# Optimization experiments

Hardware: AMD Instinct MI355X
Metric: run time of the kernel (lower is better)

## Reference

```python
import jax, jax.numpy as jnp
import numpy as np

DIM = 1024

def setup_inputs() -> dict:
    key = jax.random.key(0)
    k1, k2, k3, k4, k5 = jax.random.split(key, 5)
    B, S, D = 32, 2048, DIM
    hidden_state = jax.random.normal(k1, (B, D), dtype=jnp.float32)
    encoder_outputs = jax.random.normal(k2, (B, S, D), dtype=jnp.float32)
    # linear1: (2D -> D) with bias; linear2: (D -> 1) no bias
    W1 = jax.random.normal(k3, (2 * D, D), dtype=jnp.float32) / np.sqrt(2 * D)
    b1 = jnp.zeros((D,), dtype=jnp.float32)
    w2 = jax.random.normal(k4, (D,), dtype=jnp.float32) / np.sqrt(D)
    return {"hidden_state": hidden_state, "encoder_outputs": encoder_outputs,
            "W1": W1, "b1": b1, "w2": w2}

def reference(hidden_state, encoder_outputs, W1, b1, w2):
    B, S, D = encoder_outputs.shape
    # concat(encoder_outputs, broadcast hidden) @ W1 == enc @ W1_enc + hid @ W1_hid
    W1_enc, W1_hid = W1[:D], W1[D:]                      # each [D, D]
    enc_proj = jnp.einsum('bsd,de->bse', encoder_outputs, W1_enc)
    hid_proj = jnp.einsum('bd,de->be', hidden_state, W1_hid)
    h = jnp.tanh(enc_proj + hid_proj[:, None, :] + b1)    # [B, S, D]
    e = jnp.einsum('bsd,d->bs', h, w2)                    # [B, S]
    alpha = jax.nn.softmax(e, axis=1)                     # [B, S]
    context = jnp.einsum('bs,bsd->bd', alpha, encoder_outputs)  # [B, D]
    return context
```

## Files before the change

### kernel.cpp

```cpp
#include <hip/hip_runtime.h>
#include <hip/hip_bf16.h>
#include <cstdint>

typedef __bf16 bf16;
typedef __bf16 bf16x8 __attribute__((ext_vector_type(8)));
typedef float  f32x4  __attribute__((ext_vector_type(4)));

#define N_ENCB   0u
#define N_W1BT   134217728u
#define N_C      136314880u
#define N_E      136445952u
#define N_ALPHA  136707072u
#define N_HIDP   136968192u
#define N_CTXP   138016768u
#define N_TOTAL  140113920ull

#define O_W1BT   0u
#define O_C      2097152u
#define O_E      2228224u
#define O_ALPHA  2490368u
#define O_HIDP   2752512u
#define O_CTXP   3801088u

__global__ void k_convert(const float* __restrict__ in, bf16* __restrict__ out) {
    size_t i = ((size_t)blockIdx.x * 256 + threadIdx.x) * 8;
    const size_t stride = (size_t)2048 * 256 * 8;
    for (; i < 67108864ull; i += stride) {
        f32x4 a = *(const f32x4*)(in + i);
        f32x4 b = *(const f32x4*)(in + i + 4);
        bf16x8 o;
        o[0]=(bf16)a[0]; o[1]=(bf16)a[1]; o[2]=(bf16)a[2]; o[3]=(bf16)a[3];
        o[4]=(bf16)b[0]; o[5]=(bf16)b[1]; o[6]=(bf16)b[2]; o[7]=(bf16)b[3];
        *(bf16x8*)(out + i) = o;
    }
}

__global__ void k_cvec_init(const float* __restrict__ b1, float* __restrict__ cvec) {
    int i = blockIdx.x * 256 + threadIdx.x;
    cvec[i] = b1[i & 1023];
}

__global__ void k_hid_atomic(const float* __restrict__ hid, const float* __restrict__ W1,
                             float* __restrict__ cvec) {
    int e = blockIdx.x * 256 + threadIdx.x;
    int dch = blockIdx.y;
    float acc[32];
#pragma unroll
    for (int b = 0; b < 32; ++b) acc[b] = 0.f;
    int d0 = dch * 32;
#pragma unroll 4
    for (int dd = 0; dd < 32; ++dd) {
        int d = d0 + dd;
        float w = W1[(size_t)(1024 + d) * 1024 + e];
#pragma unroll
        for (int b = 0; b < 32; ++b) acc[b] += hid[b * 1024 + d] * w;
    }
#pragma unroll
    for (int b = 0; b < 32; ++b) atomicAdd(&cvec[b * 1024 + e], acc[b]);
}

__global__ void k_hid_partial(const float* __restrict__ hid, const float* __restrict__ W1,
                              float* __restrict__ hidp) {
    int e = blockIdx.x * 256 + threadIdx.x;
    int dch = blockIdx.y;
    float acc[32];
#pragma unroll
    for (int b = 0; b < 32; ++b) acc[b] = 0.f;
    int d0 = dch * 128;
    for (int dd = 0; dd < 128; ++dd) {
        int d = d0 + dd;
        float w = W1[(size_t)(1024 + d) * 1024 + e];
#pragma unroll
        for (int b = 0; b < 32; ++b) acc[b] += hid[b * 1024 + d] * w;
    }
#pragma unroll
    for (int b = 0; b < 32; ++b) hidp[((size_t)dch * 32 + b) * 1024 + e] = acc[b];
}

__global__ void k_hid_reduce(const float* __restrict__ hidp, const float* __restrict__ b1,
                             float* __restrict__ cvec) {
    int i = blockIdx.x * 256 + threadIdx.x;
    int e = i & 1023;
    float s = b1[e];
#pragma unroll
    for (int dch = 0; dch < 8; ++dch) s += hidp[(size_t)dch * 32768 + i];
    cvec[i] = s;
}

__global__ void k_w1t(const float* __restrict__ W1, bf16* __restrict__ w1bt) {
    __shared__ float tile[32][33];
    int tx = threadIdx.x, ty = threadIdx.y;
    int bx = blockIdx.x, by = blockIdx.y;
#pragma unroll
    for (int i = 0; i < 4; ++i)
        tile[ty + i * 8][tx] = W1[(size_t)(by * 32 + ty + i * 8) * 1024 + bx * 32 + tx];
    __syncthreads();
#pragma unroll
    for (int i = 0; i < 4; ++i)
        w1bt[(size_t)(bx * 32 + ty + i * 8) * 1024 + by * 32 + tx] = (bf16)tile[tx][ty + i * 8];
}

__device__ inline float fast_tanh(float x) {
    float e2 = __expf(2.f * x);
    return 1.f - 2.f / (e2 + 1.f);
}

#define SBAR  __builtin_amdgcn_s_barrier()
#define LGKM0 asm volatile("s_waitcnt lgkmcnt(0)" ::: "memory")
#define VMC2  asm volatile("s_waitcnt vmcnt(2)" ::: "memory")
#define VMC4  asm volatile("s_waitcnt vmcnt(4)" ::: "memory")
#define PRIO1 __builtin_amdgcn_s_setprio(1)
#define PRIO0 __builtin_amdgcn_s_setprio(0)

template<int D, int MH>
__device__ __forceinline__ void rdA4(const char* p, bf16x8 (&bA)[4]) {
#pragma unroll
    for (int m = 0; m < 4; ++m)
        bA[m] = *(const bf16x8*)(p + D * 32768 + MH * 8192 + m * 2048);
}
template<int D>
__device__ __forceinline__ void rdB4(const char* p, bf16x8 (&bB)[4]) {
#pragma unroll
    for (int n = 0; n < 4; ++n)
        bB[n] = *(const bf16x8*)(p + D * 32768 + n * 2048);
}
template<int MH>
__device__ __forceinline__ void mfma16(bf16x8 (&bA)[4], bf16x8 (&bB)[4], f32x4 (&acc)[8][4]) {
#pragma unroll
    for (int m = 0; m < 4; ++m)
#pragma unroll
        for (int n = 0; n < 4; ++n)
            acc[MH * 4 + m][n] = __builtin_amdgcn_mfma_f32_16x16x32_bf16(
                bA[m], bB[n], acc[MH * 4 + m][n], 0, 0, 0);
}

__global__ __launch_bounds__(512, 1) void k_gemm8(
    const bf16* __restrict__ encb, const bf16* __restrict__ w1bt,
    const float* __restrict__ cvec, const float* __restrict__ w2,
    float* __restrict__ ebuf)
{
    __shared__ __align__(16) char smem[131072];
    const int t = threadIdx.x;
    const int lane = t & 63;
    const int w  = t >> 6;
    const int wr = w >> 2;
    const int wc = w & 3;
    const int l15 = lane & 15, g = (lane >> 4) & 3;

    unsigned bidx = blockIdx.x;
    unsigned swz0 = (bidx & 7u) * 128u + (bidx >> 3);
    const int nt  = swz0 & 3;
    const int mt0 = swz0 >> 2;
    const int n0  = nt * 256;

    const int r6  = t >> 3;
    const int gsl = (t & 7) ^ (r6 & 7);
    const char* srcA    = (const char*)encb + (size_t)(mt0 * 256 + r6) * 2048 + gsl * 16;
    const char* srcA_nx = srcA + (size_t)2048 * 2048;
    const char* srcB    = (const char*)w1bt + (size_t)(n0 + r6) * 2048 + gsl * 16;

#define STAGE_A(SRC, D, H, KT) do { \
    const char* _s = (SRC) + (size_t)(H) * 262144 + (size_t)(KT) * 128; \
    __builtin_amdgcn_global_load_lds((const __attribute__((address_space(1))) unsigned int*)_s, \
        (__attribute__((address_space(3))) unsigned int*)(smem + (D) * 32768 + (H) * 16384 + w * 1024), 16, 0, 0); \
    __builtin_amdgcn_global_load_lds((const __attribute__((address_space(1))) unsigned int*)(_s + 131072), \
        (__attribute__((address_space(3))) unsigned int*)(smem + (D) * 32768 + (H) * 16384 + 8192 + w * 1024), 16, 0, 0); \
} while (0)
#define STAGE_B(D, H, KT) do { \
    const char* _s = srcB + (size_t)(H) * 262144 + (size_t)(KT) * 128; \
    __builtin_amdgcn_global_load_lds((const __attribute__((address_space(1))) unsigned int*)_s, \
        (__attribute__((address_space(3))) unsigned int*)(smem + 65536 + (D) * 32768 + (H) * 16384 + w * 1024), 16, 0, 0); \
    __builtin_amdgcn_global_load_lds((const __attribute__((address_space(1))) unsigned int*)(_s + 131072), \
        (__attribute__((address_space(3))) unsigned int*)(smem + 65536 + (D) * 32768 + (H) * 16384 + 8192 + w * 1024), 16, 0, 0); \
} while (0)

    const int rbA = wr * 128 + l15;
    const int rbB = wc * 64 + l15;
    const int sK0 = (g ^ (l15 & 7)) << 4;
    const int sK1 = sK0 ^ 64;
    const char* pA0 = smem + rbA * 128 + sK0;
    const char* pA1 = smem + rbA * 128 + sK1;
    const char* pB0 = smem + 65536 + rbB * 128 + sK0;
    const char* pB1 = smem + 65536 + rbB * 128 + sK1;

    f32x4 acc[8][4] = {};
    bf16x8 bA[4], bB[4];

    float wv[4];
    int gcol[4];
#pragma unroll
    for (int n = 0; n < 4; ++n) {
        gcol[n] = n0 + wc * 64 + n * 16 + l15;
        wv[n] = w2[gcol[n]];
    }

    STAGE_A(srcA, 0, 0, 0); STAGE_A(srcA, 0, 1, 0);
    STAGE_B(0, 0, 0); STAGE_B(0, 1, 0);
    STAGE_B(1, 0, 1); STAGE_B(1, 1, 1);
    VMC4; SBAR;

#pragma unroll 1
    for (int j = 0; j < 4; ++j) {
#pragma unroll 1
        for (int i = 0; i < 8; ++i) {
            const int st1 = 2 * i + 1;
            const int st2 = (2 * i + 2) & 15;
            const int st3 = (2 * i + 3) & 15;
            const char* sA2 = (i == 7) ? ((j < 3) ? srcA_nx : srcA) : srcA;

            rdA4<0, 0>(pA0, bA); rdB4<0>(pB0, bB);
            STAGE_A(srcA, 1, 0, st1);
            SBAR; LGKM0; PRIO1; mfma16<0>(bA, bB, acc); PRIO0; SBAR;
            rdA4<0, 1>(pA0, bA);
            STAGE_A(srcA, 1, 1, st1);
            SBAR; LGKM0; PRIO1; mfma16<1>(bA, bB, acc); PRIO0; SBAR;
            rdA4<0, 0>(pA1, bA); rdB4<0>(pB1, bB);
            SBAR; LGKM0; PRIO1; mfma16<0>(bA, bB, acc); PRIO0; SBAR;
            rdA4<0, 1>(pA1, bA);
            STAGE_B(0, 0, st2);
            SBAR; LGKM0; PRIO1; mfma16<1>(bA, bB, acc); PRIO0; VMC2; SBAR;
            rdA4<1, 0>(pA0, bA); rdB4<1>(pB0, bB);
            STAGE_B(0, 1, st2);
            SBAR; LGKM0; PRIO1; mfma16<0>(bA, bB, acc); PRIO0; SBAR;
            rdA4<1, 1>(pA0, bA);
            STAGE_A(sA2, 0, 0, st2);
            SBAR; LGKM0; PRIO1; mfma16<1>(bA, bB, acc); PRIO0; SBAR;
            rdA4<1, 0>(pA1, bA); rdB4<1>(pB1, bB);
            STAGE_A(sA2, 0, 1, st2);
            SBAR; LGKM0; PRIO1; mfma16<0>(bA, bB, acc); PRIO0; SBAR;
            rdA4<1, 1>(pA1, bA);
            STAGE_B(1, 0, st3); STAGE_B(1, 1, st3);
            SBAR; LGKM0; PRIO1; mfma16<1>(bA, bB, acc); PRIO0; VMC4; SBAR;
        }

        const int m0j = (mt0 + 8 * j) * 256;
        const int bj  = m0j >> 11;
        float cv[4];
#pragma unroll
        for (int n = 0; n < 4; ++n) cv[n] = cvec[bj * 1024 + gcol[n]];
#pragma unroll
        for (int m = 0; m < 8; ++m) {
#pragma unroll
            for (int r = 0; r < 4; ++r) {
                float s = 0.f;
#pragma unroll
                for (int n = 0; n < 4; ++n)
                    s += fast_tanh(acc[m][n][r] + cv[n]) * wv[n];
                s += __shfl_xor(s, 1); s += __shfl_xor(s, 2);
                s += __shfl_xor(s, 4); s += __shfl_xor(s, 8);
                if (l15 == 0)
                    atomicAdd(&ebuf[m0j + wr * 128 + m * 16 + g * 4 + r], s);
            }
        }
#pragma unroll
        for (int m = 0; m < 8; ++m)
#pragma unroll
            for (int n = 0; n < 4; ++n)
                acc[m][n] = f32x4{0.f, 0.f, 0.f, 0.f};

        srcA = srcA_nx;
        srcA_nx += (size_t)2048 * 2048;
    }
#undef STAGE_A
#undef STAGE_B
}

__global__ __launch_bounds__(256, 3) void k_gemm_e(
    const float* __restrict__ enc, const bf16* __restrict__ w1bt,
    const float* __restrict__ cvec, const float* __restrict__ w2,
    float* __restrict__ ebuf)
{
    __shared__ __align__(16) unsigned char smem[24 * 1024];
    const int t = threadIdx.x;
    const int lane = t & 63;
    const int w = t >> 6;
    const int wr = w >> 1, wc = w & 1;
    const int l15 = lane & 15, g = lane >> 4;

    unsigned raw = blockIdx.x;
    unsigned swz = (raw & 7u) * 512u + (raw >> 3);
    const int nt = swz & 7, mt = swz >> 3;
    const int m0 = mt * 128, n0 = nt * 128;
    const int b = m0 >> 11;

    int rowA = (t >> 3);
    int slotA = (t & 7) ^ (rowA & 7);
    const char* gA0 = (const char*)enc + (size_t)(m0 + rowA) * 4096 + slotA * 16;
    int rowB = (t >> 2);
    int slotB = (t & 3) ^ ((t >> 3) & 3);
    const char* gB0 = (const char*)w1bt + (size_t)(n0 + rowB) * 2048 + slotB * 16;

    int rowA0 = wr * 64 + l15;
    unsigned offA0 = (unsigned)rowA0 * 128 + ((((2 * g)) ^ (l15 & 7)) << 4);
    int rowB0 = wc * 64 + l15;
    unsigned offB0 = 16384u + (unsigned)rowB0 * 64 + (((g ^ ((l15 >> 1) & 3))) << 4);

    f32x4 acc[4][4] = {};

    for (int kt = 0; kt < 32; ++kt) {
        const char* pa = gA0 + kt * 128;
        const char* pb = gB0 + kt * 64;
#pragma unroll
        for (int c = 0; c < 4; ++c)
            __builtin_amdgcn_global_load_lds(
                (const __attribute__((address_space(1))) unsigned int*)(pa + (size_t)c * 131072),
                (__attribute__((address_space(3))) unsigned int*)(smem + c * 4096 + w * 1024), 16, 0, 0);
#pragma unroll
        for (int c = 0; c < 2; ++c)
            __builtin_amdgcn_global_load_lds(
                (const __attribute__((address_space(1))) unsigned int*)(pb + (size_t)c * 131072),
                (__attribute__((address_space(3))) unsigned int*)(smem + 16384 + c * 4096 + w * 1024), 16, 0, 0);
        __syncthreads();

        bf16x8 af[4], bfr[4];
#pragma unroll
        for (int m = 0; m < 4; ++m) {
            unsigned o0 = offA0 + m * 2048;
            f32x4 lo = *(const f32x4*)(smem + o0);
            f32x4 hi = *(const f32x4*)(smem + (o0 ^ 16u));
            bf16x8 a;
            a[0] = (bf16)lo[0]; a[1] = (bf16)lo[1]; a[2] = (bf16)lo[2]; a[3] = (bf16)lo[3];
            a[4] = (bf16)hi[0]; a[5] = (bf16)hi[1]; a[6] = (bf16)hi[2]; a[7] = (bf16)hi[3];
            af[m] = a;
        }
#pragma unroll
        for (int n = 0; n < 4; ++n)
            bfr[n] = *(const bf16x8*)(smem + (offB0 + n * 1024));
#pragma unroll
        for (int m = 0; m < 4; ++m)
#pragma unroll
            for (int n = 0; n < 4; ++n)
                acc[m][n] = __builtin_amdgcn_mfma_f32_16x16x32_bf16(af[m], bfr[n], acc[m][n], 0, 0, 0);
        __syncthreads();
    }

    float cv[4], wv[4];
#pragma unroll
    for (int n = 0; n < 4; ++n) {
        int gcol = n0 + wc * 64 + n * 16 + l15;
        cv[n] = cvec[b * 1024 + gcol];
        wv[n] = w2[gcol];
    }
#pragma unroll
    for (int m = 0; m < 4; ++m) {
#pragma unroll
        for (int r = 0; r < 4; ++r) {
            float s = 0.f;
#pragma unroll
            for (int n = 0; n < 4; ++n)
                s += fast_tanh(acc[m][n][r] + cv[n]) * wv[n];
            s += __shfl_xor(s, 1); s += __shfl_xor(s, 2);
            s += __shfl_xor(s, 4); s += __shfl_xor(s, 8);
            if (l15 == 0)
                atomicAdd(&ebuf[m0 + wr * 64 + m * 16 + g * 4 + r], s);
        }
    }
}

__global__ void k_softmax(const float* __restrict__ ebuf, float* __restrict__ alpha) {
    int bb = blockIdx.x, t = threadIdx.x;
    __shared__ float red[4], red2[4];
    float v[8];
    float mx = -1e30f;
#pragma unroll
    for (int i = 0; i < 8; ++i) { v[i] = ebuf[bb * 2048 + i * 256 + t]; mx = fmaxf(mx, v[i]); }
    for (int o = 32; o > 0; o >>= 1) mx = fmaxf(mx, __shfl_xor(mx, o));
    if ((t & 63) == 0) red[t >> 6] = mx;
    __syncthreads();
    mx = fmaxf(fmaxf(red[0], red[1]), fmaxf(red[2], red[3]));
    float sum = 0.f;
#pragma unroll
    for (int i = 0; i < 8; ++i) { v[i] = __expf(v[i] - mx); sum += v[i]; }
    for (int o = 32; o > 0; o >>= 1) sum += __shfl_xor(sum, o);
    if ((t & 63) == 0) red2[t >> 6] = sum;
    __syncthreads();
    sum = red2[0] + red2[1] + red2[2] + red2[3];
    float inv = 1.f / sum;
#pragma unroll
    for (int i = 0; i < 8; ++i) alpha[bb * 2048 + i * 256 + t] = v[i] * inv;
}

__global__ void k_ctx_partial_b(const bf16* __restrict__ encb, const float* __restrict__ alpha,
                                float* __restrict__ ctxp) {
    int bid = blockIdx.x;
    int bb = bid >> 4, sc = bid & 15;
    int t = threadIdx.x;
    __shared__ float al[128];
    __shared__ float red[128 * 8];
    if (t < 128) al[t] = alpha[bb * 2048 + sc * 128 + t];
    __syncthreads();
    int d0 = (t & 127) * 8;
    int sp = t >> 7;
    float acc[8] = {};
    const bf16* base = encb + ((size_t)bb * 2048 + sc * 128 + sp) * 1024 + d0;
    for (int s = 0; s < 128; s += 2) {
        bf16x8 v = *(const bf16x8*)(base + (size_t)s * 1024);
        float a = al[s + sp];
#pragma unroll
        for (int k = 0; k < 8; ++k) acc[k] += a * (float)v[k];
    }
    if (sp == 1) {
#pragma unroll
        for (int k = 0; k < 8; ++k) red[(t & 127) * 8 + k] = acc[k];
    }
    __syncthreads();
    if (sp == 0) {
        float* o = ctxp + (size_t)bid * 1024 + d0;
#pragma unroll
        for (int k = 0; k < 8; ++k) o[k] = acc[k] + red[t * 8 + k];
    }
}

__global__ void k_ctx_partial(const float* __restrict__ enc, const float* __restrict__ alpha,
                              float* __restrict__ ctxp) {
    int bid = blockIdx.x;
    int bb = bid >> 4, sc = bid & 15;
    int t = threadIdx.x;
    __shared__ float al[128];
    if (t < 128) al[t] = alpha[bb * 2048 + sc * 128 + t];
    __syncthreads();
    f32x4 acc = {0.f, 0.f, 0.f, 0.f};
    const f32x4* base = (const f32x4*)(enc + ((size_t)bb * 2048 + sc * 128) * 1024) + t;
    for (int s = 0; s < 128; ++s) {
        f32x4 vv = base[(size_t)s * 256];
        acc += vv * al[s];
    }
    *((f32x4*)(ctxp + (size_t)bid * 1024) + t) = acc;
}

__global__ void k_ctx_reduce(const float* __restrict__ ctxp, float* __restrict__ out) {
    int i = blockIdx.x * 256 + threadIdx.x;
    int bb = i >> 10, d = i & 1023;
    float s = 0.f;
#pragma unroll
    for (int sc = 0; sc < 16; ++sc) s += ctxp[((size_t)(bb * 16 + sc)) * 1024 + d];
    out[i] = s;
}

extern "C" void kernel_launch(void* const* d_in, const int* in_sizes, int n_in,
                              void* d_out, int out_size, void* d_ws, size_t ws_size,
                              hipStream_t stream) {
    const float* hid = (const float*)d_in[0];
    const float* enc = (const float*)d_in[1];
    const float* W1  = (const float*)d_in[2];
    const float* b1  = (const float*)d_in[3];
    const float* w2  = (const float*)d_in[4];
    float* out = (float*)d_out;
    char* ws = (char*)d_ws;

    if (ws_size >= N_TOTAL) {
        bf16*  encb  = (bf16*)(ws + N_ENCB);
        bf16*  w1bt  = (bf16*)(ws + N_W1BT);
        float* cvec  = (float*)(ws + N_C);
        float* ebuf  = (float*)(ws + N_E);
        float* alpha = (float*)(ws + N_ALPHA);
        float* ctxp  = (float*)(ws + N_CTXP);

        hipMemsetAsync(ebuf, 0, 65536 * sizeof(float), stream);
        k_convert<<<2048, 256, 0, stream>>>(enc, encb);
        k_w1t<<<dim3(32, 32), dim3(32, 8), 0, stream>>>(W1, w1bt);
        k_cvec_init<<<128, 256, 0, stream>>>(b1, cvec);
        k_hid_atomic<<<dim3(4, 32), 256, 0, stream>>>(hid, W1, cvec);
        k_gemm8<<<256, 512, 0, stream>>>(encb, w1bt, cvec, w2, ebuf);
        k_softmax<<<32, 256, 0, stream>>>(ebuf, alpha);
        k_ctx_partial_b<<<512, 256, 0, stream>>>(encb, alpha, ctxp);
        k_ctx_reduce<<<128, 256, 0, stream>>>(ctxp, out);
    } else {
        bf16*  w1bt  = (bf16*)(ws + O_W1BT);
        float* cvec  = (float*)(ws + O_C);
        float* ebuf  = (float*)(ws + O_E);
        float* alpha = (float*)(ws + O_ALPHA);
        float* hidp  = (float*)(ws + O_HIDP);
        float* ctxp  = (float*)(ws + O_CTXP);

        hipMemsetAsync(ebuf, 0, 65536 * sizeof(float), stream);
        k_hid_partial<<<dim3(4, 8), 256, 0, stream>>>(hid, W1, hidp);
        k_w1t<<<dim3(32, 32), dim3(32, 8), 0, stream>>>(W1, w1bt);
        k_hid_reduce<<<128, 256, 0, stream>>>(hidp, b1, cvec);
        k_gemm_e<<<4096, 256, 0, stream>>>(enc, w1bt, cvec, w2, ebuf);
        k_softmax<<<32, 256, 0, stream>>>(ebuf, alpha);
        k_ctx_partial<<<512, 256, 0, stream>>>(enc, alpha, ctxp);
        k_ctx_reduce<<<128, 256, 0, stream>>>(ctxp, out);
    }
}
```

Measured before the change: 267.0 us.

## Convert encoder outputs into pre-tiled swizzled bf16 layout for contiguous GEMM staging

Replaces the flat fp32-to-bf16 conversion with a kernel that transposes encoder outputs through LDS into a tile-major, XOR-swizzled layout. Each 256-row by 128-byte K-slice is then contiguous, so the GEMM's global-to-LDS A loads read contiguous 16-byte chunks per thread instead of strided rows. The context kernel is rewritten to read the new layout. The aim is better DRAM and cache locality for the A-operand loads, at the cost of a more complex conversion kernel that uses 128KB of LDS per block and so runs at low occupancy.

```diff
diff --git a/kernel.cpp b/kernel.cpp
--- a/kernel.cpp
+++ b/kernel.cpp
@@ -3,10 +3,11 @@
 #include <cstdint>
 
 typedef __bf16 bf16;
+typedef __bf16 bf16x4 __attribute__((ext_vector_type(4)));
 typedef __bf16 bf16x8 __attribute__((ext_vector_type(8)));
 typedef float  f32x4  __attribute__((ext_vector_type(4)));
 
-#define N_ENCB   0u
+#define N_ENCT   0u
 #define N_W1BT   134217728u
 #define N_C      136314880u
 #define N_E      136445952u
@@ -22,16 +23,29 @@
 #define O_HIDP   2752512u
 #define O_CTXP   3801088u
 
-__global__ void k_convert(const float* __restrict__ in, bf16* __restrict__ out) {
-    size_t i = ((size_t)blockIdx.x * 256 + threadIdx.x) * 8;
-    const size_t stride = (size_t)2048 * 256 * 8;
-    for (; i < 67108864ull; i += stride) {
-        f32x4 a = *(const f32x4*)(in + i);
-        f32x4 b = *(const f32x4*)(in + i + 4);
-        bf16x8 o;
-        o[0]=(bf16)a[0]; o[1]=(bf16)a[1]; o[2]=(bf16)a[2]; o[3]=(bf16)a[3];
-        o[4]=(bf16)b[0]; o[5]=(bf16)b[1]; o[6]=(bf16)b[2]; o[7]=(bf16)b[3];
-        *(bf16x8*)(out + i) = o;
+__global__ __launch_bounds__(256) void k_convT(const float* __restrict__ in,
+                                               bf16* __restrict__ encT) {
+    __shared__ __align__(16) char lds[131072];
+    const int t = threadIdx.x;
+    const int mtg = blockIdx.x >> 2, q = blockIdx.x & 3;
+    const float* src = in + (size_t)(mtg * 256 + q * 64) * 1024;
+#pragma unroll 8
+    for (int p = 0; p < 64; ++p) {
+        f32x4 v = *(const f32x4*)(src + (size_t)p * 1024 + t * 4);
+        bf16x4 o;
+        o[0] = (bf16)v[0]; o[1] = (bf16)v[1]; o[2] = (bf16)v[2]; o[3] = (bf16)v[3];
+        *(bf16x4*)(lds + p * 2048 + ((t * 8) ^ ((p & 7) << 4))) = o;
+    }
+    __syncthreads();
+    char* dstb = (char*)encT + (size_t)mtg * 524288 + (size_t)q * 64 * 128;
+#pragma unroll 2
+    for (int kt = 0; kt < 16; ++kt) {
+#pragma unroll
+        for (int h = 0; h < 2; ++h) {
+            int r = h * 32 + (t >> 3);
+            f32x4 val = *(const f32x4*)(lds + r * 2048 + kt * 128 + (t & 7) * 16);
+            *(f32x4*)(dstb + (size_t)kt * 32768 + r * 128 + (t & 7) * 16) = val;
+        }
     }
 }
 
@@ -135,7 +149,7 @@
 }
 
 __global__ __launch_bounds__(512, 1) void k_gemm8(
-    const bf16* __restrict__ encb, const bf16* __restrict__ w1bt,
+    const bf16* __restrict__ encT, const bf16* __restrict__ w1bt,
     const float* __restrict__ cvec, const float* __restrict__ w2,
     float* __restrict__ ebuf)
 {
@@ -155,15 +169,14 @@
 
     const int r6  = t >> 3;
     const int gsl = (t & 7) ^ (r6 & 7);
-    const char* srcA    = (const char*)encb + (size_t)(mt0 * 256 + r6) * 2048 + gsl * 16;
-    const char* srcA_nx = srcA + (size_t)2048 * 2048;
-    const char* srcB    = (const char*)w1bt + (size_t)(n0 + r6) * 2048 + gsl * 16;
-
-#define STAGE_A(SRC, D, H, KT) do { \
-    const char* _s = (SRC) + (size_t)(H) * 262144 + (size_t)(KT) * 128; \
+    const char* tbAj = (const char*)encT + (size_t)mt0 * 524288;
+    const char* srcB = (const char*)w1bt + (size_t)(n0 + r6) * 2048 + gsl * 16;
+
+#define STAGE_A(TB, D, H, KT) do { \
+    const char* _s = (TB) + (size_t)(KT) * 32768 + (H) * 16384 + t * 16; \
     __builtin_amdgcn_global_load_lds((const __attribute__((address_space(1))) unsigned int*)_s, \
         (__attribute__((address_space(3))) unsigned int*)(smem + (D) * 32768 + (H) * 16384 + w * 1024), 16, 0, 0); \
-    __builtin_amdgcn_global_load_lds((const __attribute__((address_space(1))) unsigned int*)(_s + 131072), \
+    __builtin_amdgcn_global_load_lds((const __attribute__((address_space(1))) unsigned int*)(_s + 8192), \
         (__attribute__((address_space(3))) unsigned int*)(smem + (D) * 32768 + (H) * 16384 + 8192 + w * 1024), 16, 0, 0); \
 } while (0)
 #define STAGE_B(D, H, KT) do { \
@@ -194,7 +207,7 @@
         wv[n] = w2[gcol[n]];
     }
 
-    STAGE_A(srcA, 0, 0, 0); STAGE_A(srcA, 0, 1, 0);
+    STAGE_A(tbAj, 0, 0, 0); STAGE_A(tbAj, 0, 1, 0);
     STAGE_B(0, 0, 0); STAGE_B(0, 1, 0);
     STAGE_B(1, 0, 1); STAGE_B(1, 1, 1);
     VMC4; SBAR;
@@ -206,13 +219,13 @@
             const int st1 = 2 * i + 1;
             const int st2 = (2 * i + 2) & 15;
             const int st3 = (2 * i + 3) & 15;
-            const char* sA2 = (i == 7) ? ((j < 3) ? srcA_nx : srcA) : srcA;
+            const char* tb2 = (i == 7) ? ((j < 3) ? tbAj + 4194304 : tbAj) : tbAj;
 
             rdA4<0, 0>(pA0, bA); rdB4<0>(pB0, bB);
-            STAGE_A(srcA, 1, 0, st1);
+            STAGE_A(tbAj, 1, 0, st1);
             SBAR; LGKM0; PRIO1; mfma16<0>(bA, bB, acc); PRIO0; SBAR;
             rdA4<0, 1>(pA0, bA);
-            STAGE_A(srcA, 1, 1, st1);
+            STAGE_A(tbAj, 1, 1, st1);
             SBAR; LGKM0; PRIO1; mfma16<1>(bA, bB, acc); PRIO0; SBAR;
             rdA4<0, 0>(pA1, bA); rdB4<0>(pB1, bB);
             SBAR; LGKM0; PRIO1; mfma16<0>(bA, bB, acc); PRIO0; SBAR;
@@ -223,10 +236,10 @@
             STAGE_B(0, 1, st2);
             SBAR; LGKM0; PRIO1; mfma16<0>(bA, bB, acc); PRIO0; SBAR;
             rdA4<1, 1>(pA0, bA);
-            STAGE_A(sA2, 0, 0, st2);
+            STAGE_A(tb2, 0, 0, st2);
             SBAR; LGKM0; PRIO1; mfma16<1>(bA, bB, acc); PRIO0; SBAR;
             rdA4<1, 0>(pA1, bA); rdB4<1>(pB1, bB);
-            STAGE_A(sA2, 0, 1, st2);
+            STAGE_A(tb2, 0, 1, st2);
             SBAR; LGKM0; PRIO1; mfma16<0>(bA, bB, acc); PRIO0; SBAR;
             rdA4<1, 1>(pA1, bA);
             STAGE_B(1, 0, st3); STAGE_B(1, 1, st3);
@@ -258,8 +271,7 @@
             for (int n = 0; n < 4; ++n)
                 acc[m][n] = f32x4{0.f, 0.f, 0.f, 0.f};
 
-        srcA = srcA_nx;
-        srcA_nx += (size_t)2048 * 2048;
+        tbAj += 4194304;
     }
 #undef STAGE_A
 #undef STAGE_B
@@ -380,34 +392,36 @@
     for (int i = 0; i < 8; ++i) alpha[bb * 2048 + i * 256 + t] = v[i] * inv;
 }
 
-__global__ void k_ctx_partial_b(const bf16* __restrict__ encb, const float* __restrict__ alpha,
-                                float* __restrict__ ctxp) {
+__global__ void k_ctx_t(const bf16* __restrict__ encT, const float* __restrict__ alpha,
+                        float* __restrict__ ctxp) {
     int bid = blockIdx.x;
     int bb = bid >> 4, sc = bid & 15;
     int t = threadIdx.x;
     __shared__ float al[128];
-    __shared__ float red[128 * 8];
+    __shared__ float red[1024];
     if (t < 128) al[t] = alpha[bb * 2048 + sc * 128 + t];
     __syncthreads();
-    int d0 = (t & 127) * 8;
-    int sp = t >> 7;
+    int j = t & 127, kt = j >> 3, sL = j & 7, sp = t >> 7;
+    int mtg = bb * 8 + (sc >> 1);
+    int rbase = (sc & 1) * 128;
+    const char* base = (const char*)encT + (size_t)mtg * 524288 + (size_t)kt * 32768;
     float acc[8] = {};
-    const bf16* base = encb + ((size_t)bb * 2048 + sc * 128 + sp) * 1024 + d0;
-    for (int s = 0; s < 128; s += 2) {
-        bf16x8 v = *(const bf16x8*)(base + (size_t)s * 1024);
-        float a = al[s + sp];
+    for (int ri = 0; ri < 64; ++ri) {
+        int rr = rbase + ri * 2 + sp;
+        bf16x8 v = *(const bf16x8*)(base + rr * 128 + ((sL ^ (rr & 7)) << 4));
+        float a = al[ri * 2 + sp];
 #pragma unroll
         for (int k = 0; k < 8; ++k) acc[k] += a * (float)v[k];
     }
     if (sp == 1) {
 #pragma unroll
-        for (int k = 0; k < 8; ++k) red[(t & 127) * 8 + k] = acc[k];
+        for (int k = 0; k < 8; ++k) red[j * 8 + k] = acc[k];
     }
     __syncthreads();
     if (sp == 0) {
-        float* o = ctxp + (size_t)bid * 1024 + d0;
-#pragma unroll
-        for (int k = 0; k < 8; ++k) o[k] = acc[k] + red[t * 8 + k];
+        float* o = ctxp + (size_t)bid * 1024 + j * 8;
+#pragma unroll
+        for (int k = 0; k < 8; ++k) o[k] = acc[k] + red[j * 8 + k];
     }
 }
 
@@ -449,7 +463,7 @@
     char* ws = (char*)d_ws;
 
     if (ws_size >= N_TOTAL) {
-        bf16*  encb  = (bf16*)(ws + N_ENCB);
+        bf16*  encT  = (bf16*)(ws + N_ENCT);
         bf16*  w1bt  = (bf16*)(ws + N_W1BT);
         float* cvec  = (float*)(ws + N_C);
         float* ebuf  = (float*)(ws + N_E);
@@ -457,13 +471,13 @@
         float* ctxp  = (float*)(ws + N_CTXP);
 
         hipMemsetAsync(ebuf, 0, 65536 * sizeof(float), stream);
-        k_convert<<<2048, 256, 0, stream>>>(enc, encb);
+        k_convT<<<1024, 256, 0, stream>>>(enc, encT);
         k_w1t<<<dim3(32, 32), dim3(32, 8), 0, stream>>>(W1, w1bt);
         k_cvec_init<<<128, 256, 0, stream>>>(b1, cvec);
         k_hid_atomic<<<dim3(4, 32), 256, 0, stream>>>(hid, W1, cvec);
-        k_gemm8<<<256, 512, 0, stream>>>(encb, w1bt, cvec, w2, ebuf);
+        k_gemm8<<<256, 512, 0, stream>>>(encT, w1bt, cvec, w2, ebuf);
         k_softmax<<<32, 256, 0, stream>>>(ebuf, alpha);
-        k_ctx_partial_b<<<512, 256, 0, stream>>>(encb, alpha, ctxp);
+        k_ctx_t<<<512, 256, 0, stream>>>(encT, alpha, ctxp);
         k_ctx_reduce<<<128, 256, 0, stream>>>(ctxp, out);
     } else {
         bf16*  w1bt  = (bf16*)(ws + O_W1BT);
```

Result: slower. 281.2 us (+5.3%).

## Fuse fp32-to-bf16 encoder conversion into the GEMM A-tile staging

Applied to the files above, without the earlier changes.

Removes the separate k_convert pass. The GEMM now loads fp32 encoder rows into registers, converts them to bf16, writes them into swizzled LDS, and has the nt==0 blocks also write the bf16 copy to global memory for the later context kernel. This saves one full read and write pass over the 256MB encoder tensor. In exchange, the GEMM reads twice as many bytes for A, and A staging goes from async direct-to-LDS loads to register loads and LDS stores, which adds VGPR pressure and changes the pipeline's wait structure.

```diff
diff --git a/kernel.cpp b/kernel.cpp
--- a/kernel.cpp
+++ b/kernel.cpp
@@ -11,7 +11,6 @@
 #define N_C      136314880u
 #define N_E      136445952u
 #define N_ALPHA  136707072u
-#define N_HIDP   136968192u
 #define N_CTXP   138016768u
 #define N_TOTAL  140113920ull
 
@@ -22,19 +21,6 @@
 #define O_HIDP   2752512u
 #define O_CTXP   3801088u
 
-__global__ void k_convert(const float* __restrict__ in, bf16* __restrict__ out) {
-    size_t i = ((size_t)blockIdx.x * 256 + threadIdx.x) * 8;
-    const size_t stride = (size_t)2048 * 256 * 8;
-    for (; i < 67108864ull; i += stride) {
-        f32x4 a = *(const f32x4*)(in + i);
-        f32x4 b = *(const f32x4*)(in + i + 4);
-        bf16x8 o;
-        o[0]=(bf16)a[0]; o[1]=(bf16)a[1]; o[2]=(bf16)a[2]; o[3]=(bf16)a[3];
-        o[4]=(bf16)b[0]; o[5]=(bf16)b[1]; o[6]=(bf16)b[2]; o[7]=(bf16)b[3];
-        *(bf16x8*)(out + i) = o;
-    }
-}
-
 __global__ void k_cvec_init(const float* __restrict__ b1, float* __restrict__ cvec) {
     int i = blockIdx.x * 256 + threadIdx.x;
     cvec[i] = b1[i & 1023];
@@ -105,39 +91,38 @@
     return 1.f - 2.f / (e2 + 1.f);
 }
 
-#define SBAR  __builtin_amdgcn_s_barrier()
-#define LGKM0 asm volatile("s_waitcnt lgkmcnt(0)" ::: "memory")
-#define VMC2  asm volatile("s_waitcnt vmcnt(2)" ::: "memory")
-#define VMC4  asm volatile("s_waitcnt vmcnt(4)" ::: "memory")
-#define PRIO1 __builtin_amdgcn_s_setprio(1)
-#define PRIO0 __builtin_amdgcn_s_setprio(0)
+#define SBAR   __builtin_amdgcn_s_barrier()
+#define LGKM0  asm volatile("s_waitcnt lgkmcnt(0)" ::: "memory")
+#define VMC4   asm volatile("s_waitcnt vmcnt(4)" ::: "memory")
+#define PRIO1  __builtin_amdgcn_s_setprio(1)
+#define PRIO0  __builtin_amdgcn_s_setprio(0)
 
 template<int D, int MH>
-__device__ __forceinline__ void rdA4(const char* p, bf16x8 (&bA)[4]) {
+__device__ __forceinline__ void rdA4(const char* p, bf16x8 (&o)[4]) {
 #pragma unroll
     for (int m = 0; m < 4; ++m)
-        bA[m] = *(const bf16x8*)(p + D * 32768 + MH * 8192 + m * 2048);
+        o[m] = *(const bf16x8*)(p + D * 32768 + MH * 8192 + m * 2048);
 }
 template<int D>
-__device__ __forceinline__ void rdB4(const char* p, bf16x8 (&bB)[4]) {
+__device__ __forceinline__ void rdB4(const char* p, bf16x8 (&o)[4]) {
 #pragma unroll
     for (int n = 0; n < 4; ++n)
-        bB[n] = *(const bf16x8*)(p + D * 32768 + n * 2048);
+        o[n] = *(const bf16x8*)(p + D * 32768 + n * 2048);
 }
 template<int MH>
-__device__ __forceinline__ void mfma16(bf16x8 (&bA)[4], bf16x8 (&bB)[4], f32x4 (&acc)[8][4]) {
+__device__ __forceinline__ void mfma16(bf16x8 (&fa)[4], bf16x8 (&fb)[4], f32x4 (&acc)[8][4]) {
 #pragma unroll
     for (int m = 0; m < 4; ++m)
 #pragma unroll
         for (int n = 0; n < 4; ++n)
             acc[MH * 4 + m][n] = __builtin_amdgcn_mfma_f32_16x16x32_bf16(
-                bA[m], bB[n], acc[MH * 4 + m][n], 0, 0, 0);
+                fa[m], fb[n], acc[MH * 4 + m][n], 0, 0, 0);
 }
 
 __global__ __launch_bounds__(512, 1) void k_gemm8(
-    const bf16* __restrict__ encb, const bf16* __restrict__ w1bt,
+    const float* __restrict__ encf, const bf16* __restrict__ w1bt,
     const float* __restrict__ cvec, const float* __restrict__ w2,
-    float* __restrict__ ebuf)
+    float* __restrict__ ebuf, bf16* __restrict__ encb)
 {
     __shared__ __align__(16) char smem[131072];
     const int t = threadIdx.x;
@@ -152,20 +137,50 @@
     const int nt  = swz0 & 3;
     const int mt0 = swz0 >> 2;
     const int n0  = nt * 256;
+    const bool wb = (nt == 0);
+
+    const int arow = t >> 2;
+    const int r7   = arow & 7;
+    const int l0   = ((t & 3) * 2) ^ r7;
+    const int l1   = ((t & 3) * 2 + 1) ^ r7;
+
+    const float* srcAf    = encf + (size_t)mt0 * 256 * 1024;
+    const float* srcAf_nx = srcAf + (size_t)2048 * 1024;
+    bf16* wbase    = encb + (size_t)mt0 * 256 * 1024;
+    bf16* wbase_nx = wbase + (size_t)2048 * 1024;
+    const float* baseA0 = srcAf;
+    bf16*        wb0    = wbase;
 
     const int r6  = t >> 3;
     const int gsl = (t & 7) ^ (r6 & 7);
-    const char* srcA    = (const char*)encb + (size_t)(mt0 * 256 + r6) * 2048 + gsl * 16;
-    const char* srcA_nx = srcA + (size_t)2048 * 2048;
-    const char* srcB    = (const char*)w1bt + (size_t)(n0 + r6) * 2048 + gsl * 16;
-
-#define STAGE_A(SRC, D, H, KT) do { \
-    const char* _s = (SRC) + (size_t)(H) * 262144 + (size_t)(KT) * 128; \
-    __builtin_amdgcn_global_load_lds((const __attribute__((address_space(1))) unsigned int*)_s, \
-        (__attribute__((address_space(3))) unsigned int*)(smem + (D) * 32768 + (H) * 16384 + w * 1024), 16, 0, 0); \
-    __builtin_amdgcn_global_load_lds((const __attribute__((address_space(1))) unsigned int*)(_s + 131072), \
-        (__attribute__((address_space(3))) unsigned int*)(smem + (D) * 32768 + (H) * 16384 + 8192 + w * 1024), 16, 0, 0); \
+    const char* srcB = (const char*)w1bt + (size_t)(n0 + r6) * 2048 + gsl * 16;
+
+    f32x4 ra0, ra1, ra2, ra3;
+
+#define ISSUE_A(BASE, KT, H) do { \
+    const float* _r = (BASE) + (size_t)((H) * 128 + arow) * 1024 + (KT) * 64; \
+    ra0 = *(const f32x4*)(_r + l0 * 8); \
+    ra1 = *(const f32x4*)(_r + l0 * 8 + 4); \
+    ra2 = *(const f32x4*)(_r + l1 * 8); \
+    ra3 = *(const f32x4*)(_r + l1 * 8 + 4); \
 } while (0)
+
+#define WRITE_A(D, H, WBASE, KT) do { \
+    bf16x8 _p0, _p1; \
+    _p0[0]=(bf16)ra0[0]; _p0[1]=(bf16)ra0[1]; _p0[2]=(bf16)ra0[2]; _p0[3]=(bf16)ra0[3]; \
+    _p0[4]=(bf16)ra1[0]; _p0[5]=(bf16)ra1[1]; _p0[6]=(bf16)ra1[2]; _p0[7]=(bf16)ra1[3]; \
+    _p1[0]=(bf16)ra2[0]; _p1[1]=(bf16)ra2[1]; _p1[2]=(bf16)ra2[2]; _p1[3]=(bf16)ra2[3]; \
+    _p1[4]=(bf16)ra3[0]; _p1[5]=(bf16)ra3[1]; _p1[6]=(bf16)ra3[2]; _p1[7]=(bf16)ra3[3]; \
+    char* _w = smem + (D) * 32768 + (H) * 16384 + t * 32; \
+    *(bf16x8*)_w = _p0; \
+    *(bf16x8*)(_w + 16) = _p1; \
+    if (wb) { \
+        bf16* _g = (WBASE) + (size_t)((H) * 128 + arow) * 1024 + (KT) * 64; \
+        *(bf16x8*)(_g + l0 * 8) = _p0; \
+        *(bf16x8*)(_g + l1 * 8) = _p1; \
+    } \
+} while (0)
+
 #define STAGE_B(D, H, KT) do { \
     const char* _s = srcB + (size_t)(H) * 262144 + (size_t)(KT) * 128; \
     __builtin_amdgcn_global_load_lds((const __attribute__((address_space(1))) unsigned int*)_s, \
@@ -184,7 +199,7 @@
     const char* pB1 = smem + 65536 + rbB * 128 + sK1;
 
     f32x4 acc[8][4] = {};
-    bf16x8 bA[4], bB[4];
+    bf16x8 fa[4], fb[4];
 
     float wv[4];
     int gcol[4];
@@ -194,43 +209,55 @@
         wv[n] = w2[gcol[n]];
     }
 
-    STAGE_A(srcA, 0, 0, 0); STAGE_A(srcA, 0, 1, 0);
+    ISSUE_A(srcAf, 0, 0);
+    WRITE_A(0, 0, wbase, 0);
+    ISSUE_A(srcAf, 0, 1);
+    WRITE_A(0, 1, wbase, 0);
     STAGE_B(0, 0, 0); STAGE_B(0, 1, 0);
     STAGE_B(1, 0, 1); STAGE_B(1, 1, 1);
-    VMC4; SBAR;
+    VMC4;
+    ISSUE_A(srcAf, 1, 0);
+    LGKM0;
+    SBAR;
 
 #pragma unroll 1
     for (int j = 0; j < 4; ++j) {
 #pragma unroll 1
         for (int i = 0; i < 8; ++i) {
             const int st1 = 2 * i + 1;
-            const int st2 = (2 * i + 2) & 15;
-            const int st3 = (2 * i + 3) & 15;
-            const char* sA2 = (i == 7) ? ((j < 3) ? srcA_nx : srcA) : srcA;
-
-            rdA4<0, 0>(pA0, bA); rdB4<0>(pB0, bB);
-            STAGE_A(srcA, 1, 0, st1);
-            SBAR; LGKM0; PRIO1; mfma16<0>(bA, bB, acc); PRIO0; SBAR;
-            rdA4<0, 1>(pA0, bA);
-            STAGE_A(srcA, 1, 1, st1);
-            SBAR; LGKM0; PRIO1; mfma16<1>(bA, bB, acc); PRIO0; SBAR;
-            rdA4<0, 0>(pA1, bA); rdB4<0>(pB1, bB);
-            SBAR; LGKM0; PRIO1; mfma16<0>(bA, bB, acc); PRIO0; SBAR;
-            rdA4<0, 1>(pA1, bA);
+            const int st2 = (i == 7) ? 0 : 2 * i + 2;
+            const int st3 = (i == 7) ? 1 : 2 * i + 3;
+            const bool lastI = (i == 7);
+            const float* fA2 = lastI ? ((j < 3) ? srcAf_nx : baseA0) : srcAf;
+            bf16*        wb2 = lastI ? ((j < 3) ? wbase_nx : wb0)   : wbase;
+
+            WRITE_A(1, 0, wbase, st1);
+            ISSUE_A(srcAf, st1, 1);
+            rdA4<0, 0>(pA0, fa); rdB4<0>(pB0, fb);
+            SBAR; LGKM0; PRIO1; mfma16<0>(fa, fb, acc); PRIO0; SBAR;
+            WRITE_A(1, 1, wbase, st1);
+            rdA4<0, 1>(pA0, fa);
+            SBAR; LGKM0; PRIO1; mfma16<1>(fa, fb, acc); PRIO0; SBAR;
+            rdA4<0, 0>(pA1, fa); rdB4<0>(pB1, fb);
+            SBAR; LGKM0; PRIO1; mfma16<0>(fa, fb, acc); PRIO0; SBAR;
             STAGE_B(0, 0, st2);
-            SBAR; LGKM0; PRIO1; mfma16<1>(bA, bB, acc); PRIO0; VMC2; SBAR;
-            rdA4<1, 0>(pA0, bA); rdB4<1>(pB0, bB);
+            rdA4<0, 1>(pA1, fa);
+            SBAR; LGKM0; PRIO1; mfma16<1>(fa, fb, acc); PRIO0; SBAR;
+            ISSUE_A(fA2, st2, 0);
             STAGE_B(0, 1, st2);
-            SBAR; LGKM0; PRIO1; mfma16<0>(bA, bB, acc); PRIO0; SBAR;
-            rdA4<1, 1>(pA0, bA);
-            STAGE_A(sA2, 0, 0, st2);
-            SBAR; LGKM0; PRIO1; mfma16<1>(bA, bB, acc); PRIO0; SBAR;
-            rdA4<1, 0>(pA1, bA); rdB4<1>(pB1, bB);
-            STAGE_A(sA2, 0, 1, st2);
-            SBAR; LGKM0; PRIO1; mfma16<0>(bA, bB, acc); PRIO0; SBAR;
-            rdA4<1, 1>(pA1, bA);
+            rdA4<1, 0>(pA0, fa); rdB4<1>(pB0, fb);
+            SBAR; LGKM0; PRIO1; mfma16<0>(fa, fb, acc); PRIO0; SBAR;
+            WRITE_A(0, 0, wb2, st2);
+            ISSUE_A(fA2, st2, 1);
+            rdA4<1, 1>(pA0, fa);
+            SBAR; LGKM0; PRIO1; mfma16<1>(fa, fb, acc); PRIO0; SBAR;
+            WRITE_A(0, 1, wb2, st2);
+            rdA4<1, 0>(pA1, fa); rdB4<1>(pB1, fb);
+            SBAR; LGKM0; PRIO1; mfma16<0>(fa, fb, acc); PRIO0; SBAR;
+            ISSUE_A((lastI ? ((j < 3) ? srcAf_nx : baseA0) : srcAf), st3, 0);
             STAGE_B(1, 0, st3); STAGE_B(1, 1, st3);
-            SBAR; LGKM0; PRIO1; mfma16<1>(bA, bB, acc); PRIO0; VMC4; SBAR;
+            rdA4<1, 1>(pA1, fa);
+            SBAR; LGKM0; PRIO1; mfma16<1>(fa, fb, acc); PRIO0; SBAR;
         }
 
         const int m0j = (mt0 + 8 * j) * 256;
@@ -258,10 +285,11 @@
             for (int n = 0; n < 4; ++n)
                 acc[m][n] = f32x4{0.f, 0.f, 0.f, 0.f};
 
-        srcA = srcA_nx;
-        srcA_nx += (size_t)2048 * 2048;
-    }
-#undef STAGE_A
+        srcAf = srcAf_nx; srcAf_nx += (size_t)2048 * 1024;
+        wbase = wbase_nx; wbase_nx += (size_t)2048 * 1024;
+    }
+#undef ISSUE_A
+#undef WRITE_A
 #undef STAGE_B
 }
 
@@ -457,11 +485,10 @@
         float* ctxp  = (float*)(ws + N_CTXP);
 
         hipMemsetAsync(ebuf, 0, 65536 * sizeof(float), stream);
-        k_convert<<<2048, 256, 0, stream>>>(enc, encb);
         k_w1t<<<dim3(32, 32), dim3(32, 8), 0, stream>>>(W1, w1bt);
         k_cvec_init<<<128, 256, 0, stream>>>(b1, cvec);
         k_hid_atomic<<<dim3(4, 32), 256, 0, stream>>>(hid, W1, cvec);
-        k_gemm8<<<256, 512, 0, stream>>>(encb, w1bt, cvec, w2, ebuf);
+        k_gemm8<<<256, 512, 0, stream>>>(enc, w1bt, cvec, w2, ebuf, encb);
         k_softmax<<<32, 256, 0, stream>>>(ebuf, alpha);
         k_ctx_partial_b<<<512, 256, 0, stream>>>(encb, alpha, ctxp);
         k_ctx_reduce<<<128, 256, 0, stream>>>(ctxp, out);
```

New measurement: 353.4 us. 1.32x slower.
